# Kernel tuning notes

Hardware: AMD Instinct MI355X
Metric: run time of the kernel (lower is better)

## Reference

```python
import jax, jax.numpy as jnp
import numpy as np
from jax import lax

FPS_NUM, K = 2048, 32


def fps_subsample(x, n):
    # x: [B, N, 3] -> [B, n, 3]; farthest point sampling, deterministic start at index 0
    B, N, _ = x.shape
    d0 = jnp.sum((x - x[:, :1]) ** 2, axis=-1)  # [B, N] dist to point 0

    def step(dists, _):
        nxt = jnp.argmax(dists, axis=1)                       # [B]
        p = x[jnp.arange(B), nxt]                             # [B, 3]
        dists = jnp.minimum(dists, jnp.sum((x - p[:, None]) ** 2, axis=-1))
        return dists, nxt

    _, idxs = lax.scan(step, d0, None, length=n - 1)          # [n-1, B]
    idxs = jnp.concatenate([jnp.zeros((1, B), jnp.int32), idxs.astype(jnp.int32)], axis=0).T  # [B, n]
    return x[jnp.arange(B)[:, None], idxs]                    # [B, n, 3]


def knn_idx(x, k):
    # x: [B, C, N] -> [B, N, k] indices of k nearest neighbors in feature space
    xx = jnp.sum(x * x, axis=1)                               # [B, N]
    inner = jnp.einsum('bcn,bcm->bnm', x, x)
    neg_dist = 2.0 * inner - xx[:, :, None] - xx[:, None, :]  # -||xi-xj||^2
    return lax.top_k(neg_dist, k)[1]


def get_graph_feature(x, k):
    # DGCNN edge features: x [B, C, N] -> [B, 2C, N, k]
    B, C, N = x.shape
    idx = knn_idx(x, k)                                       # [B, N, k]
    xt = jnp.transpose(x, (0, 2, 1))                          # [B, N, C]
    nbr = xt[jnp.arange(B)[:, None, None], idx]               # [B, N, k, C]
    ctr = jnp.broadcast_to(xt[:, :, None], nbr.shape)
    feat = jnp.concatenate([nbr - ctr, ctr], axis=-1)         # [B, N, k, 2C]
    return jnp.transpose(feat, (0, 3, 1, 2))


def attention(xq, xk, pos, Wq, bq, Wk, bk, Wv, bv, Wp, bp):
    # positional attention over k neighbors: xq/xk [B, Cin, N, k], pos [B, 3, N] -> [B, dim, N]
    q = jnp.einsum('bcnk,dc->bdnk', xq, Wq) + bq[:, None, None]
    kk = jnp.einsum('bcnk,dc->bdnk', xk, Wk) + bk[:, None, None]
    v = jnp.einsum('bcnk,dc->bdnk', xk, Wv) + bv[:, None, None]
    p = jnp.einsum('bcn,dc->bdn', pos, Wp) + bp[:, None]      # [B, dim, N]
    dim = Wq.shape[0]
    logits = jnp.einsum('bdnk,bdnk->bnk', q, kk) / jnp.sqrt(jnp.float32(dim))
    attn = jax.nn.softmax(logits, axis=-1)                    # [B, N, k]
    return jnp.einsum('bnk,bdnk->bdn', attn, v + p[:, :, :, None])


def _layer_params(key, cin, dim):
    ks = jax.random.split(key, 4)
    s = 1.0 / np.sqrt(cin)
    return (jax.random.normal(ks[0], (dim, cin), jnp.float32) * s,
            jnp.zeros((dim,), jnp.float32),
            jax.random.normal(ks[1], (dim, cin), jnp.float32) * s,
            jnp.zeros((dim,), jnp.float32),
            jax.random.normal(ks[2], (dim, cin), jnp.float32) * s,
            jnp.zeros((dim,), jnp.float32),
            jax.random.normal(ks[3], (dim, 3), jnp.float32) * (1.0 / np.sqrt(3.0)),
            jnp.zeros((dim,), jnp.float32))


def setup_inputs() -> dict:
    key = jax.random.key(0)
    kx, k1, k2, k3 = jax.random.split(key, 4)
    x = jax.random.normal(kx, (8, 16384, 3), jnp.float32)
    out = {'x': x}
    for name, kk_, cin, dim in (('t1', k1, 6, 64), ('t2', k2, 128, 64), ('t3', k3, 128, 128)):
        Wq, bq, Wk, bk, Wv, bv, Wp, bp = _layer_params(kk_, cin, dim)
        out.update({f'{name}_Wq': Wq, f'{name}_bq': bq, f'{name}_Wk': Wk, f'{name}_bk': bk,
                    f'{name}_Wv': Wv, f'{name}_bv': bv, f'{name}_Wp': Wp, f'{name}_bp': bp})
    return out


def reference(x, t1_Wq, t1_bq, t1_Wk, t1_bk, t1_Wv, t1_bv, t1_Wp, t1_bp,
              t2_Wq, t2_bq, t2_Wk, t2_bk, t2_Wv, t2_bv, t2_Wp, t2_bp,
              t3_Wq, t3_bq, t3_Wk, t3_bk, t3_Wv, t3_bv, t3_Wp, t3_bp):
    partial = jnp.transpose(fps_subsample(x, FPS_NUM), (0, 2, 1))       # [B, 3, n]
    g = get_graph_feature(partial, K)                                    # [B, 6, n, k]
    x1 = attention(g, g, partial, t1_Wq, t1_bq, t1_Wk, t1_bk, t1_Wv, t1_bv, t1_Wp, t1_bp)  # [B, 64, n]
    g = get_graph_feature(x1, K)                                         # [B, 128, n, k]
    x2 = attention(g, g, partial, t2_Wq, t2_bq, t2_Wk, t2_bk, t2_Wv, t2_bv, t2_Wp, t2_bp)  # [B, 64, n]
    g = get_graph_feature(x2, K)                                         # [B, 128, n, k]
    x3 = attention(g, g, partial, t3_Wq, t3_bq, t3_Wk, t3_bk, t3_Wv, t3_bv, t3_Wp, t3_bp)  # [B, 128, n]
    feats = jnp.concatenate([x1, x2, x3], axis=1)                        # [B, 256, n]
    return jnp.concatenate([jnp.max(feats, axis=-1), jnp.mean(feats, axis=-1)], axis=1)    # [B, 512]
```

## Files before the change

### kernel.cpp

```cpp
#include <hip/hip_runtime.h>
#include <math.h>

#define NB 8
#define NIN 16384
#define NP 2048
#define KNN 32
#define TOTPTS (NB * NP)

#define NEG_INF (-__builtin_inff())

template <int CTRL, int RMASK>
__device__ __forceinline__ void dpp_amax_step(float& bv, int& bi) {
  float ov = __int_as_float(__builtin_amdgcn_update_dpp(
      __float_as_int(NEG_INF), __float_as_int(bv), CTRL, RMASK, 0xf, false));
  int oi = __builtin_amdgcn_update_dpp(0, bi, CTRL, RMASK, 0xf, false);
  if (ov > bv || (ov == bv && oi < bi)) { bv = ov; bi = oi; }
}

__device__ __forceinline__ void wave_amax63(float& bv, int& bi) {
  dpp_amax_step<0x111, 0xf>(bv, bi);
  dpp_amax_step<0x112, 0xf>(bv, bi);
  dpp_amax_step<0x114, 0xf>(bv, bi);
  dpp_amax_step<0x118, 0xf>(bv, bi);
  dpp_amax_step<0x142, 0xa>(bv, bi);
  dpp_amax_step<0x143, 0xc>(bv, bi);
}

__global__ __launch_bounds__(1024) void fps_kernel(const float* __restrict__ x,
                                                   float* __restrict__ partial) {
  const int b = blockIdx.x;
  const int t = threadIdx.x;
  const float* xb = x + (size_t)b * NIN * 3;
  float* pb = partial + (size_t)b * NP * 3;
  __shared__ unsigned long long skey[NP];
  for (int i = t; i < NP; i += 1024) skey[i] = 0ull;

  float2 px[8], py[8], pz[8], dd[8];
#pragma unroll
  for (int j = 0; j < 8; ++j) {
    const int i0 = (2 * j) * 1024 + t, i1 = (2 * j + 1) * 1024 + t;
    px[j] = make_float2(xb[3 * i0], xb[3 * i1]);
    py[j] = make_float2(xb[3 * i0 + 1], xb[3 * i1 + 1]);
    pz[j] = make_float2(xb[3 * i0 + 2], xb[3 * i1 + 2]);
  }
  float qx = xb[0], qy = xb[1], qz = xb[2];
  if (t == 0) { pb[0] = qx; pb[1] = qy; pb[2] = qz; }

  float bv = NEG_INF;
  int bi = 0;
#pragma unroll
  for (int j = 0; j < 8; ++j) {
    float dx = __fsub_rn(px[j].x, qx), dy = __fsub_rn(py[j].x, qy), dz = __fsub_rn(pz[j].x, qz);
    dd[j].x = __fadd_rn(__fadd_rn(__fmul_rn(dx, dx), __fmul_rn(dy, dy)), __fmul_rn(dz, dz));
    if (dd[j].x > bv) { bv = dd[j].x; bi = (2 * j) * 1024 + t; }
    dx = __fsub_rn(px[j].y, qx); dy = __fsub_rn(py[j].y, qy); dz = __fsub_rn(pz[j].y, qz);
    dd[j].y = __fadd_rn(__fadd_rn(__fmul_rn(dx, dx), __fmul_rn(dy, dy)), __fmul_rn(dz, dz));
    if (dd[j].y > bv) { bv = dd[j].y; bi = (2 * j + 1) * 1024 + t; }
  }
  __syncthreads();

  for (int it = 1; it < NP; ++it) {
    wave_amax63(bv, bi);
    if ((t & 63) == 63) {
      const unsigned long long key =
          ((unsigned long long)__float_as_uint(bv) << 32) | (unsigned int)(~bi);
      atomicMax(&skey[it], key);
    }
    __syncthreads();
    const unsigned long long gk = skey[it];
    const int gbi = (int)(~(unsigned int)gk);
    const int u = __builtin_amdgcn_readfirstlane(gbi);
    const float nqx = xb[3 * u], nqy = xb[3 * u + 1], nqz = xb[3 * u + 2];
    if (t == 0) { pb[3 * it] = nqx; pb[3 * it + 1] = nqy; pb[3 * it + 2] = nqz; }

    bv = NEG_INF;
    bi = 0;
#pragma unroll
    for (int j = 0; j < 8; ++j) {
      float dx = __fsub_rn(px[j].x, nqx), dy = __fsub_rn(py[j].x, nqy), dz = __fsub_rn(pz[j].x, nqz);
      float nd = __fadd_rn(__fadd_rn(__fmul_rn(dx, dx), __fmul_rn(dy, dy)), __fmul_rn(dz, dz));
      dd[j].x = fminf(dd[j].x, nd);
      if (dd[j].x > bv) { bv = dd[j].x; bi = (2 * j) * 1024 + t; }
      dx = __fsub_rn(px[j].y, nqx); dy = __fsub_rn(py[j].y, nqy); dz = __fsub_rn(pz[j].y, nqz);
      nd = __fadd_rn(__fadd_rn(__fmul_rn(dx, dx), __fmul_rn(dy, dy)), __fmul_rn(dz, dz));
      dd[j].y = fminf(dd[j].y, nd);
      if (dd[j].y > bv) { bv = dd[j].y; bi = (2 * j + 1) * 1024 + t; }
    }
  }
}

__global__ void xx_kernel(const float* __restrict__ F, float* __restrict__ xxg, int C) {
  int i = blockIdx.x * 256 + threadIdx.x;
  if (i >= TOTPTS) return;
  const float* f = F + (size_t)i * C;
  float s = 0.f;
  for (int c = 0; c < C; ++c) s = __fadd_rn(s, __fmul_rn(f[c], f[c]));
  xxg[i] = s;
}

template <int C>
__global__ __launch_bounds__(256) void dist_gemm(const float* __restrict__ F,
                                                 const float* __restrict__ xxg,
                                                 float* __restrict__ D, int bofs) {
  __shared__ float As[64][C + 1];
  __shared__ float Bs[64][C + 1];
  const int b = bofs + blockIdx.z;
  float* Ds = D + (size_t)blockIdx.z * NP * NP;
  const int tid = threadIdx.x;
  const int n0 = blockIdx.y * 64, m0 = blockIdx.x * 64;
  const float* Fb = F + (size_t)b * NP * C;
  const float* xxb = xxg + b * NP;
  for (int t = tid; t < 64 * C; t += 256) {
    int r = t / C, c = t - r * C;
    As[r][c] = Fb[(size_t)(n0 + r) * C + c];
    Bs[r][c] = Fb[(size_t)(m0 + r) * C + c];
  }
  __syncthreads();
  const int tx = tid & 15, ty = tid >> 4;
  float acc[4][4] = {};
  for (int c = 0; c < C; ++c) {
    float a[4], bb[4];
#pragma unroll
    for (int i = 0; i < 4; ++i) a[i] = As[ty * 4 + i][c];
#pragma unroll
    for (int j = 0; j < 4; ++j) bb[j] = Bs[tx * 4 + j][c];
#pragma unroll
    for (int i = 0; i < 4; ++i)
#pragma unroll
      for (int j = 0; j < 4; ++j) acc[i][j] = fmaf(a[i], bb[j], acc[i][j]);
  }
#pragma unroll
  for (int i = 0; i < 4; ++i) {
    int n = n0 + ty * 4 + i;
    float xn = xxb[n];
    float4 o;
    o.x = __fsub_rn(__fsub_rn(2.0f * acc[i][0], xn), xxb[m0 + tx * 4 + 0]);
    o.y = __fsub_rn(__fsub_rn(2.0f * acc[i][1], xn), xxb[m0 + tx * 4 + 1]);
    o.z = __fsub_rn(__fsub_rn(2.0f * acc[i][2], xn), xxb[m0 + tx * 4 + 2]);
    o.w = __fsub_rn(__fsub_rn(2.0f * acc[i][3], xn), xxb[m0 + tx * 4 + 3]);
    *(float4*)&Ds[(size_t)n * NP + m0 + tx * 4] = o;
  }
}

__global__ __launch_bounds__(256) void select_kernel(const float* __restrict__ D,
                                                     int* __restrict__ idxg, int bofs) {
  const int lane = threadIdx.x & 63;
  const int b = bofs + blockIdx.z;
  const int row = blockIdx.x * 4 + (threadIdx.x >> 6);
  const float* Drow = D + (size_t)blockIdx.z * NP * NP + (size_t)row * NP;
  float v[32];
#pragma unroll
  for (int s = 0; s < 32; ++s) v[s] = Drow[s * 64 + lane];
  int* out = idxg + ((size_t)b * NP + row) * KNN;
  for (int t = 0; t < KNN; ++t) {
    float bv = v[0];
    int bs = 0;
#pragma unroll
    for (int s = 1; s < 32; ++s) {
      if (v[s] > bv) { bv = v[s]; bs = s; }
    }
    int bi = bs * 64 + lane;
    wave_amax63(bv, bi);
    const int wbi = __builtin_amdgcn_readlane(bi, 63);
    if (lane == 0) out[t] = wbi;
    const bool own = (lane == (wbi & 63));
    const int cs = wbi >> 6;
#pragma unroll
    for (int s = 0; s < 32; ++s)
      if (own && s == cs) v[s] = NEG_INF;
  }
}

template <int C, int DIM>
__global__ __launch_bounds__(256) void proj_kernel(
    const float* __restrict__ F, const float* __restrict__ pos,
    const float* __restrict__ Wq, const float* __restrict__ bq,
    const float* __restrict__ Wk, const float* __restrict__ bk,
    const float* __restrict__ Wv, const float* __restrict__ bv,
    const float* __restrict__ Wp, const float* __restrict__ bp,
    float* __restrict__ Uq, float* __restrict__ Uk, float* __restrict__ Uv,
    float* __restrict__ Uqc, float* __restrict__ Ukc, float* __restrict__ W6) {
  constexpr int PTS = 16;
  constexpr int GROUPS = 256 / DIM;
  constexpr int PPT = PTS / GROUPS;
  __shared__ float xs[PTS][C];
  __shared__ float ps[PTS][3];
  const int tid = threadIdx.x;
  const int base = blockIdx.x * PTS;
  for (int t = tid; t < PTS * C; t += 256) {
    int r = t / C;
    xs[r][t - r * C] = F[(size_t)(base + r) * C + (t - r * C)];
  }
  for (int t = tid; t < PTS * 3; t += 256) {
    int r = t / 3;
    ps[r][t - r * 3] = pos[(size_t)(base + r) * 3 + (t - r * 3)];
  }
  __syncthreads();
  const int g = tid / DIM;
  const int d = tid - g * DIM;
  float uq[PPT], uqd[PPT], uk[PPT], ukd[PPT], uv[PPT], uvd[PPT];
#pragma unroll
  for (int p = 0; p < PPT; ++p) { uq[p] = uqd[p] = uk[p] = ukd[p] = uv[p] = uvd[p] = 0.f; }
  const float* wqr = Wq + (size_t)d * (2 * C);
  const float* wkr = Wk + (size_t)d * (2 * C);
  const float* wvr = Wv + (size_t)d * (2 * C);
  for (int c = 0; c < C; ++c) {
    const float wq1 = wqr[c], wqd_ = wqr[C + c] - wq1;
    const float wk1 = wkr[c], wkd_ = wkr[C + c] - wk1;
    const float wv1 = wvr[c], wvd_ = wvr[C + c] - wv1;
#pragma unroll
    for (int p = 0; p < PPT; ++p) {
      const float xc = xs[g + p * GROUPS][c];
      uq[p] = fmaf(wq1, xc, uq[p]);
      uqd[p] = fmaf(wqd_, xc, uqd[p]);
      uk[p] = fmaf(wk1, xc, uk[p]);
      ukd[p] = fmaf(wkd_, xc, ukd[p]);
      uv[p] = fmaf(wv1, xc, uv[p]);
      uvd[p] = fmaf(wvd_, xc, uvd[p]);
    }
  }
  const float bqd = bq[d], bkd = bk[d], bvd = bv[d];
  const float wp0 = Wp[d * 3], wp1 = Wp[d * 3 + 1], wp2 = Wp[d * 3 + 2], bpd = bp[d];
#pragma unroll
  for (int p = 0; p < PPT; ++p) {
    const int lp = g + p * GROUPS;
    const size_t o = (size_t)(base + lp) * DIM + d;
    const float pd = wp0 * ps[lp][0] + wp1 * ps[lp][1] + wp2 * ps[lp][2] + bpd;
    Uq[o] = uq[p];
    Uqc[o] = uqd[p] + bqd;
    Uk[o] = uk[p];
    Ukc[o] = ukd[p] + bkd;
    Uv[o] = uv[p];
    W6[o] = uvd[p] + bvd + pd;
  }
}

template <int DIM>
__global__ __launch_bounds__(256) void attn_kernel(
    const float* __restrict__ Uq, const float* __restrict__ Uk, const float* __restrict__ Uv,
    const float* __restrict__ Uqc, const float* __restrict__ Ukc, const float* __restrict__ W6g,
    const int* __restrict__ idxg, float* __restrict__ outF) {
  const int w = threadIdx.x >> 6, lane = threadIdx.x & 63;
  const int pt = blockIdx.x * 4 + w;
  const int b = pt >> 11;
  __shared__ int sidx[4][KNN];
  __shared__ float sqc[4][DIM], skc[4][DIM], sw6[4][DIM];
  __shared__ float sattn[4][KNN];
  const size_t rowo = (size_t)pt * DIM;
  if (lane < KNN) sidx[w][lane] = idxg[(size_t)pt * KNN + lane];
  for (int d = lane; d < DIM; d += 64) {
    sqc[w][d] = Uqc[rowo + d];
    skc[w][d] = Ukc[rowo + d];
    sw6[w][d] = W6g[rowo + d];
  }
  __syncthreads();
  if (lane < KNN) {
    const int ik = sidx[w][lane];
    const float* qr = Uq + (size_t)(b * NP + ik) * DIM;
    const float* kr = Uk + (size_t)(b * NP + ik) * DIM;
    float lg = 0.f;
    for (int d = 0; d < DIM; d += 4) {
      float4 qa = *(const float4*)(qr + d);
      float4 ka = *(const float4*)(kr + d);
      float4 qc = *(const float4*)(&sqc[w][d]);
      float4 kc = *(const float4*)(&skc[w][d]);
      lg += (qa.x + qc.x) * (ka.x + kc.x);
      lg += (qa.y + qc.y) * (ka.y + kc.y);
      lg += (qa.z + qc.z) * (ka.z + kc.z);
      lg += (qa.w + qc.w) * (ka.w + kc.w);
    }
    lg /= sqrtf((float)DIM);
    float m = lg;
#pragma unroll
    for (int off = 16; off; off >>= 1) m = fmaxf(m, __shfl_xor(m, off));
    float e = expf(lg - m);
    float s = e;
#pragma unroll
    for (int off = 16; off; off >>= 1) s += __shfl_xor(s, off);
    sattn[w][lane] = e / s;
  }
  __syncthreads();
  float acc[DIM / 64];
#pragma unroll
  for (int q = 0; q < DIM / 64; ++q) acc[q] = 0.f;
  for (int k = 0; k < KNN; ++k) {
    const int ik = sidx[w][k];
    const float a = sattn[w][k];
    const float* vr = Uv + (size_t)(b * NP + ik) * DIM;
#pragma unroll
    for (int q = 0; q < DIM / 64; ++q) {
      const int d = q * 64 + lane;
      acc[q] = fmaf(a, vr[d] + sw6[w][d], acc[q]);
    }
  }
#pragma unroll
  for (int q = 0; q < DIM / 64; ++q) outF[rowo + q * 64 + lane] = acc[q];
}

__global__ __launch_bounds__(256) void pool_kernel(const float* __restrict__ x1,
                                                   const float* __restrict__ x2,
                                                   const float* __restrict__ x3,
                                                   float* __restrict__ out) {
  const int b = blockIdx.x, c = threadIdx.x;
  const float* src;
  int dim, cl;
  if (c < 64) {
    src = x1 + (size_t)b * NP * 64; dim = 64; cl = c;
  } else if (c < 128) {
    src = x2 + (size_t)b * NP * 64; dim = 64; cl = c - 64;
  } else {
    src = x3 + (size_t)b * NP * 128; dim = 128; cl = c - 128;
  }
  float mx = NEG_INF, sm = 0.f;
#pragma unroll 8
  for (int n = 0; n < NP; ++n) {
    float v = src[(size_t)n * dim + cl];
    mx = fmaxf(mx, v);
    sm += v;
  }
  out[b * 512 + c] = mx;
  out[b * 512 + 256 + c] = sm * (1.0f / 2048.0f);
}

extern "C" void kernel_launch(void* const* d_in, const int* in_sizes, int n_in,
                              void* d_out, int out_size, void* d_ws, size_t ws_size,
                              hipStream_t stream) {
  const float* x = (const float*)d_in[0];
  const float* W[24];
  for (int i = 0; i < 24; ++i) W[i] = (const float*)d_in[1 + i];

  float* ws = (float*)d_ws;
  size_t off = 0;
  float* partial = ws + off; off += (size_t)NB * NP * 3;
  float* xxbuf = ws + off;   off += TOTPTS;
  int* idxb = (int*)(ws + off); off += (size_t)TOTPTS * KNN;
  float* x1 = ws + off; off += (size_t)TOTPTS * 64;
  float* x2 = ws + off; off += (size_t)TOTPTS * 64;
  float* x3 = ws + off; off += (size_t)TOTPTS * 128;
  float* Uq = ws + off;  off += (size_t)TOTPTS * 128;
  float* Uk = ws + off;  off += (size_t)TOTPTS * 128;
  float* Uv = ws + off;  off += (size_t)TOTPTS * 128;
  float* Uqc = ws + off; off += (size_t)TOTPTS * 128;
  float* Ukc = ws + off; off += (size_t)TOTPTS * 128;
  float* W6 = ws + off;  off += (size_t)TOTPTS * 128;
  if (ws_size < off * sizeof(float)) return;

  float* Dbig = ws + off;
  const size_t need_big = (off + (size_t)NB * NP * NP) * sizeof(float);
  const bool bigws = (ws_size >= need_big);
  float* D = bigws ? Dbig : Uq;
  const int NZ = bigws ? NB : 1;

  fps_kernel<<<NB, 1024, 0, stream>>>(x, partial);

  xx_kernel<<<TOTPTS / 256, 256, 0, stream>>>(partial, xxbuf, 3);
  for (int b = 0; b < NB; b += NZ) {
    dist_gemm<3><<<dim3(32, 32, NZ), 256, 0, stream>>>(partial, xxbuf, D, b);
    select_kernel<<<dim3(NP / 4, 1, NZ), 256, 0, stream>>>(D, idxb, b);
  }
  proj_kernel<3, 64><<<TOTPTS / 16, 256, 0, stream>>>(
      partial, partial, W[0], W[1], W[2], W[3], W[4], W[5], W[6], W[7],
      Uq, Uk, Uv, Uqc, Ukc, W6);
  attn_kernel<64><<<TOTPTS / 4, 256, 0, stream>>>(Uq, Uk, Uv, Uqc, Ukc, W6, idxb, x1);

  xx_kernel<<<TOTPTS / 256, 256, 0, stream>>>(x1, xxbuf, 64);
  for (int b = 0; b < NB; b += NZ) {
    dist_gemm<64><<<dim3(32, 32, NZ), 256, 0, stream>>>(x1, xxbuf, D, b);
    select_kernel<<<dim3(NP / 4, 1, NZ), 256, 0, stream>>>(D, idxb, b);
  }
  proj_kernel<64, 64><<<TOTPTS / 16, 256, 0, stream>>>(
      x1, partial, W[8], W[9], W[10], W[11], W[12], W[13], W[14], W[15],
      Uq, Uk, Uv, Uqc, Ukc, W6);
  attn_kernel<64><<<TOTPTS / 4, 256, 0, stream>>>(Uq, Uk, Uv, Uqc, Ukc, W6, idxb, x2);

  xx_kernel<<<TOTPTS / 256, 256, 0, stream>>>(x2, xxbuf, 64);
  for (int b = 0; b < NB; b += NZ) {
    dist_gemm<64><<<dim3(32, 32, NZ), 256, 0, stream>>>(x2, xxbuf, D, b);
    select_kernel<<<dim3(NP / 4, 1, NZ), 256, 0, stream>>>(D, idxb, b);
  }
  proj_kernel<64, 128><<<TOTPTS / 16, 256, 0, stream>>>(
      x2, partial, W[16], W[17], W[18], W[19], W[20], W[21], W[22], W[23],
      Uq, Uk, Uv, Uqc, Ukc, W6);
  attn_kernel<128><<<TOTPTS / 4, 256, 0, stream>>>(Uq, Uk, Uv, Uqc, Ukc, W6, idxb, x3);

  pool_kernel<<<NB, 256, 0, stream>>>(x1, x2, x3, (float*)d_out);
}
```

Measured before the change: 5.517 ms.

## Pack FPS math, split argmax reduction, GEMM-based projections, two-half attention logits

The FPS inner loop switches to packed v_pk_add/v_pk_mul float2 arithmetic, and the wave argmax becomes a float max followed by an index min instead of paired value/index DPP steps. For layers 2 and 3, the per-point projection kernel is replaced by a weight-prep kernel, a positional kernel and a tiled shared-memory GEMM that emits all six projection outputs at once. Attention logits now use all 64 lanes, each half-wave covering half the channels, and a constant replaces the sqrt divide. These changes target the serial FPS loop and the cost of the projections, at the price of extra launches, extra workspace and slightly different rounding.

```diff
diff --git a/kernel.cpp b/kernel.cpp
--- a/kernel.cpp
+++ b/kernel.cpp
@@ -9,14 +9,47 @@
 
 #define NEG_INF (-__builtin_inff())
 
+__device__ __forceinline__ float2 pk_add(float2 a, float2 b) {
+  float2 d;
+  asm("v_pk_add_f32 %0, %1, %2" : "=v"(d) : "v"(a), "v"(b));
+  return d;
+}
+__device__ __forceinline__ float2 pk_mul(float2 a, float2 b) {
+  float2 d;
+  asm("v_pk_mul_f32 %0, %1, %2" : "=v"(d) : "v"(a), "v"(b));
+  return d;
+}
+
+#define DPP_F(old, v, C, RM) \
+  __int_as_float(__builtin_amdgcn_update_dpp(__float_as_int(old), __float_as_int(v), C, RM, 0xf, false))
+#define DPP_I(old, v, C, RM) \
+  __builtin_amdgcn_update_dpp(old, v, C, RM, 0xf, false)
+
+__device__ __forceinline__ float wave_max_f(float v) {
+  v = fmaxf(v, DPP_F(NEG_INF, v, 0x111, 0xf));
+  v = fmaxf(v, DPP_F(NEG_INF, v, 0x112, 0xf));
+  v = fmaxf(v, DPP_F(NEG_INF, v, 0x114, 0xf));
+  v = fmaxf(v, DPP_F(NEG_INF, v, 0x118, 0xf));
+  v = fmaxf(v, DPP_F(NEG_INF, v, 0x142, 0xa));
+  v = fmaxf(v, DPP_F(NEG_INF, v, 0x143, 0xc));
+  return v;
+}
+__device__ __forceinline__ int wave_min_i(int v) {
+  v = min(v, DPP_I(0x7fffffff, v, 0x111, 0xf));
+  v = min(v, DPP_I(0x7fffffff, v, 0x112, 0xf));
+  v = min(v, DPP_I(0x7fffffff, v, 0x114, 0xf));
+  v = min(v, DPP_I(0x7fffffff, v, 0x118, 0xf));
+  v = min(v, DPP_I(0x7fffffff, v, 0x142, 0xa));
+  v = min(v, DPP_I(0x7fffffff, v, 0x143, 0xc));
+  return v;
+}
+
 template <int CTRL, int RMASK>
 __device__ __forceinline__ void dpp_amax_step(float& bv, int& bi) {
-  float ov = __int_as_float(__builtin_amdgcn_update_dpp(
-      __float_as_int(NEG_INF), __float_as_int(bv), CTRL, RMASK, 0xf, false));
-  int oi = __builtin_amdgcn_update_dpp(0, bi, CTRL, RMASK, 0xf, false);
+  float ov = DPP_F(NEG_INF, bv, CTRL, RMASK);
+  int oi = DPP_I(0, bi, CTRL, RMASK);
   if (ov > bv || (ov == bv && oi < bi)) { bv = ov; bi = oi; }
 }
-
 __device__ __forceinline__ void wave_amax63(float& bv, int& bi) {
   dpp_amax_step<0x111, 0xf>(bv, bi);
   dpp_amax_step<0x112, 0xf>(bv, bi);
@@ -43,27 +76,34 @@
     py[j] = make_float2(xb[3 * i0 + 1], xb[3 * i1 + 1]);
     pz[j] = make_float2(xb[3 * i0 + 2], xb[3 * i1 + 2]);
   }
-  float qx = xb[0], qy = xb[1], qz = xb[2];
-  if (t == 0) { pb[0] = qx; pb[1] = qy; pb[2] = qz; }
+  const float qx0 = xb[0], qy0 = xb[1], qz0 = xb[2];
+  if (t == 0) { pb[0] = qx0; pb[1] = qy0; pb[2] = qz0; }
 
   float bv = NEG_INF;
   int bi = 0;
-#pragma unroll
-  for (int j = 0; j < 8; ++j) {
-    float dx = __fsub_rn(px[j].x, qx), dy = __fsub_rn(py[j].x, qy), dz = __fsub_rn(pz[j].x, qz);
-    dd[j].x = __fadd_rn(__fadd_rn(__fmul_rn(dx, dx), __fmul_rn(dy, dy)), __fmul_rn(dz, dz));
-    if (dd[j].x > bv) { bv = dd[j].x; bi = (2 * j) * 1024 + t; }
-    dx = __fsub_rn(px[j].y, qx); dy = __fsub_rn(py[j].y, qy); dz = __fsub_rn(pz[j].y, qz);
-    dd[j].y = __fadd_rn(__fadd_rn(__fmul_rn(dx, dx), __fmul_rn(dy, dy)), __fmul_rn(dz, dz));
-    if (dd[j].y > bv) { bv = dd[j].y; bi = (2 * j + 1) * 1024 + t; }
+  {
+    const float2 nx2 = make_float2(-qx0, -qx0);
+    const float2 ny2 = make_float2(-qy0, -qy0);
+    const float2 nz2 = make_float2(-qz0, -qz0);
+#pragma unroll
+    for (int j = 0; j < 8; ++j) {
+      float2 dx = pk_add(px[j], nx2), dy = pk_add(py[j], ny2), dz = pk_add(pz[j], nz2);
+      float2 nd = pk_add(pk_add(pk_mul(dx, dx), pk_mul(dy, dy)), pk_mul(dz, dz));
+      dd[j] = nd;
+      if (nd.x > bv) { bv = nd.x; bi = (2 * j) * 1024 + t; }
+      if (nd.y > bv) { bv = nd.y; bi = (2 * j + 1) * 1024 + t; }
+    }
   }
   __syncthreads();
 
   for (int it = 1; it < NP; ++it) {
-    wave_amax63(bv, bi);
+    const float wm = wave_max_f(bv);
+    const float smax = __int_as_float(__builtin_amdgcn_readlane(__float_as_int(wm), 63));
+    const int sel = (bv == smax) ? bi : 0x7fffffff;
+    const int wi = wave_min_i(sel);
     if ((t & 63) == 63) {
       const unsigned long long key =
-          ((unsigned long long)__float_as_uint(bv) << 32) | (unsigned int)(~bi);
+          ((unsigned long long)__float_as_uint(smax) << 32) | (unsigned int)(~wi);
       atomicMax(&skey[it], key);
     }
     __syncthreads();
@@ -73,18 +113,21 @@
     const float nqx = xb[3 * u], nqy = xb[3 * u + 1], nqz = xb[3 * u + 2];
     if (t == 0) { pb[3 * it] = nqx; pb[3 * it + 1] = nqy; pb[3 * it + 2] = nqz; }
 
+    const float2 nx2 = make_float2(-nqx, -nqx);
+    const float2 ny2 = make_float2(-nqy, -nqy);
+    const float2 nz2 = make_float2(-nqz, -nqz);
     bv = NEG_INF;
     bi = 0;
 #pragma unroll
     for (int j = 0; j < 8; ++j) {
-      float dx = __fsub_rn(px[j].x, nqx), dy = __fsub_rn(py[j].x, nqy), dz = __fsub_rn(pz[j].x, nqz);
-      float nd = __fadd_rn(__fadd_rn(__fmul_rn(dx, dx), __fmul_rn(dy, dy)), __fmul_rn(dz, dz));
-      dd[j].x = fminf(dd[j].x, nd);
-      if (dd[j].x > bv) { bv = dd[j].x; bi = (2 * j) * 1024 + t; }
-      dx = __fsub_rn(px[j].y, nqx); dy = __fsub_rn(py[j].y, nqy); dz = __fsub_rn(pz[j].y, nqz);
-      nd = __fadd_rn(__fadd_rn(__fmul_rn(dx, dx), __fmul_rn(dy, dy)), __fmul_rn(dz, dz));
-      dd[j].y = fminf(dd[j].y, nd);
-      if (dd[j].y > bv) { bv = dd[j].y; bi = (2 * j + 1) * 1024 + t; }
+      float2 dx = pk_add(px[j], nx2), dy = pk_add(py[j], ny2), dz = pk_add(pz[j], nz2);
+      float2 nd = pk_add(pk_add(pk_mul(dx, dx), pk_mul(dy, dy)), pk_mul(dz, dz));
+      const float a0 = fminf(dd[j].x, nd.x);
+      dd[j].x = a0;
+      if (a0 > bv) { bv = a0; bi = (2 * j) * 1024 + t; }
+      const float a1 = fminf(dd[j].y, nd.y);
+      dd[j].y = a1;
+      if (a1 > bv) { bv = a1; bi = (2 * j + 1) * 1024 + t; }
     }
   }
 }
@@ -236,6 +279,87 @@
 }
 
 template <int DIM>
+__global__ void prep_kernel(const float* __restrict__ Wq, const float* __restrict__ bq,
+                            const float* __restrict__ Wk, const float* __restrict__ bk,
+                            const float* __restrict__ Wv, const float* __restrict__ bv,
+                            float* __restrict__ Wcat, float* __restrict__ bcat) {
+  const int o = blockIdx.x * 256 + threadIdx.x;
+  constexpr int ND = 6 * DIM;
+  if (o >= ND) return;
+  const int blk = o / DIM, d = o % DIM;
+  bcat[o] = (blk == 1) ? bq[d] : (blk == 3) ? bk[d] : (blk == 5) ? bv[d] : 0.f;
+  const float* W = (blk < 2) ? Wq : (blk < 4) ? Wk : Wv;
+  for (int c = 0; c < 64; ++c) {
+    const float w1 = W[(size_t)d * 128 + c];
+    const float w2 = W[(size_t)d * 128 + 64 + c];
+    Wcat[(size_t)c * ND + o] = (blk & 1) ? (w2 - w1) : w1;
+  }
+}
+
+template <int DIM>
+__global__ void pos_kernel(const float* __restrict__ pos, const float* __restrict__ Wp,
+                           const float* __restrict__ bp, float* __restrict__ P) {
+  const int idx = blockIdx.x * 256 + threadIdx.x;
+  const int pt = idx / DIM, d = idx - pt * DIM;
+  P[idx] = Wp[d * 3] * pos[pt * 3] + Wp[d * 3 + 1] * pos[pt * 3 + 1] +
+           Wp[d * 3 + 2] * pos[pt * 3 + 2] + bp[d];
+}
+
+template <int DIM>
+__global__ __launch_bounds__(256) void gemm_proj(
+    const float* __restrict__ F, const float* __restrict__ Wcat,
+    const float* __restrict__ bcat, const float* __restrict__ P,
+    float* __restrict__ Uq, float* __restrict__ Uqc, float* __restrict__ Uk,
+    float* __restrict__ Ukc, float* __restrict__ Uv, float* __restrict__ W6) {
+  constexpr int ND = 6 * DIM;
+  __shared__ float As[64][65];
+  __shared__ float Bs[64][65];
+  const int tid = threadIdx.x;
+  const int p0 = blockIdx.x * 64;
+  const int n0 = blockIdx.y * 64;
+  {
+    const int r0 = tid >> 4, c4 = (tid & 15) * 4;
+    for (int r = r0; r < 64; r += 16) {
+      float4 a = *(const float4*)&F[(size_t)(p0 + r) * 64 + c4];
+      As[r][c4] = a.x; As[r][c4 + 1] = a.y; As[r][c4 + 2] = a.z; As[r][c4 + 3] = a.w;
+      float4 bb = *(const float4*)&Wcat[(size_t)r * ND + n0 + c4];
+      Bs[r][c4] = bb.x; Bs[r][c4 + 1] = bb.y; Bs[r][c4 + 2] = bb.z; Bs[r][c4 + 3] = bb.w;
+    }
+  }
+  __syncthreads();
+  const int tx = tid & 15, ty = tid >> 4;
+  float acc[4][4] = {};
+#pragma unroll 4
+  for (int c = 0; c < 64; ++c) {
+    float a[4], bb[4];
+#pragma unroll
+    for (int i = 0; i < 4; ++i) a[i] = As[ty * 4 + i][c];
+#pragma unroll
+    for (int j = 0; j < 4; ++j) bb[j] = Bs[c][tx * 4 + j];
+#pragma unroll
+    for (int i = 0; i < 4; ++i)
+#pragma unroll
+      for (int j = 0; j < 4; ++j) acc[i][j] = fmaf(a[i], bb[j], acc[i][j]);
+  }
+  const int obuf = n0 / DIM;
+  const int oloc = n0 - obuf * DIM;
+  float* outp = (obuf == 0) ? Uq : (obuf == 1) ? Uqc : (obuf == 2) ? Uk
+              : (obuf == 3) ? Ukc : (obuf == 4) ? Uv : W6;
+  const float b0 = bcat[n0 + tx * 4], b1 = bcat[n0 + tx * 4 + 1];
+  const float b2 = bcat[n0 + tx * 4 + 2], b3 = bcat[n0 + tx * 4 + 3];
+#pragma unroll
+  for (int i = 0; i < 4; ++i) {
+    const int p = p0 + ty * 4 + i;
+    float4 r = make_float4(acc[i][0] + b0, acc[i][1] + b1, acc[i][2] + b2, acc[i][3] + b3);
+    if (obuf == 5) {
+      float4 pv = *(const float4*)&P[(size_t)p * DIM + oloc + tx * 4];
+      r.x += pv.x; r.y += pv.y; r.z += pv.z; r.w += pv.w;
+    }
+    *(float4*)&outp[(size_t)p * DIM + oloc + tx * 4] = r;
+  }
+}
+
+template <int DIM>
 __global__ __launch_bounds__(256) void attn_kernel(
     const float* __restrict__ Uq, const float* __restrict__ Uk, const float* __restrict__ Uv,
     const float* __restrict__ Uqc, const float* __restrict__ Ukc, const float* __restrict__ W6g,
@@ -254,12 +378,15 @@
     sw6[w][d] = W6g[rowo + d];
   }
   __syncthreads();
-  if (lane < KNN) {
-    const int ik = sidx[w][lane];
+  {
+    const int kk = lane & 31;
+    const int h = lane >> 5;
+    const int ik = sidx[w][kk];
     const float* qr = Uq + (size_t)(b * NP + ik) * DIM;
     const float* kr = Uk + (size_t)(b * NP + ik) * DIM;
     float lg = 0.f;
-    for (int d = 0; d < DIM; d += 4) {
+    const int d0 = h * (DIM / 2), d1 = d0 + DIM / 2;
+    for (int d = d0; d < d1; d += 4) {
       float4 qa = *(const float4*)(qr + d);
       float4 ka = *(const float4*)(kr + d);
       float4 qc = *(const float4*)(&sqc[w][d]);
@@ -269,7 +396,8 @@
       lg += (qa.z + qc.z) * (ka.z + kc.z);
       lg += (qa.w + qc.w) * (ka.w + kc.w);
     }
-    lg /= sqrtf((float)DIM);
+    lg += __shfl_xor(lg, 32);
+    lg *= (DIM == 64) ? 0.125f : 0.08838834764831845f;
     float m = lg;
 #pragma unroll
     for (int off = 16; off; off >>= 1) m = fmaxf(m, __shfl_xor(m, off));
@@ -277,7 +405,7 @@
     float s = e;
 #pragma unroll
     for (int off = 16; off; off >>= 1) s += __shfl_xor(s, off);
-    sattn[w][lane] = e / s;
+    if (lane < KNN) sattn[w][lane] = e / s;
   }
   __syncthreads();
   float acc[DIM / 64];
@@ -343,6 +471,9 @@
   float* Uqc = ws + off; off += (size_t)TOTPTS * 128;
   float* Ukc = ws + off; off += (size_t)TOTPTS * 128;
   float* W6 = ws + off;  off += (size_t)TOTPTS * 128;
+  float* Pbuf = ws + off; off += (size_t)TOTPTS * 128;
+  float* Wcat = ws + off; off += (size_t)64 * 768;
+  float* bcat = ws + off; off += 768;
   if (ws_size < off * sizeof(float)) return;
 
   float* Dbig = ws + off;
@@ -368,9 +499,10 @@
     dist_gemm<64><<<dim3(32, 32, NZ), 256, 0, stream>>>(x1, xxbuf, D, b);
     select_kernel<<<dim3(NP / 4, 1, NZ), 256, 0, stream>>>(D, idxb, b);
   }
-  proj_kernel<64, 64><<<TOTPTS / 16, 256, 0, stream>>>(
-      x1, partial, W[8], W[9], W[10], W[11], W[12], W[13], W[14], W[15],
-      Uq, Uk, Uv, Uqc, Ukc, W6);
+  prep_kernel<64><<<2, 256, 0, stream>>>(W[8], W[9], W[10], W[11], W[12], W[13], Wcat, bcat);
+  pos_kernel<64><<<TOTPTS * 64 / 256, 256, 0, stream>>>(partial, W[14], W[15], Pbuf);
+  gemm_proj<64><<<dim3(TOTPTS / 64, 6), 256, 0, stream>>>(
+      x1, Wcat, bcat, Pbuf, Uq, Uqc, Uk, Ukc, Uv, W6);
   attn_kernel<64><<<TOTPTS / 4, 256, 0, stream>>>(Uq, Uk, Uv, Uqc, Ukc, W6, idxb, x2);
 
   xx_kernel<<<TOTPTS / 256, 256, 0, stream>>>(x2, xxbuf, 64);
@@ -378,9 +510,10 @@
     dist_gemm<64><<<dim3(32, 32, NZ), 256, 0, stream>>>(x2, xxbuf, D, b);
     select_kernel<<<dim3(NP / 4, 1, NZ), 256, 0, stream>>>(D, idxb, b);
   }
-  proj_kernel<64, 128><<<TOTPTS / 16, 256, 0, stream>>>(
-      x2, partial, W[16], W[17], W[18], W[19], W[20], W[21], W[22], W[23],
-      Uq, Uk, Uv, Uqc, Ukc, W6);
+  prep_kernel<128><<<3, 256, 0, stream>>>(W[16], W[17], W[18], W[19], W[20], W[21], Wcat, bcat);
+  pos_kernel<128><<<TOTPTS * 128 / 256, 256, 0, stream>>>(partial, W[22], W[23], Pbuf);
+  gemm_proj<128><<<dim3(TOTPTS / 64, 12), 256, 0, stream>>>(
+      x2, Wcat, bcat, Pbuf, Uq, Uqc, Uk, Ukc, Uv, W6);
   attn_kernel<128><<<TOTPTS / 4, 256, 0, stream>>>(Uq, Uk, Uv, Uqc, Ukc, W6, idxb, x3);
 
   pool_kernel<<<NB, 256, 0, stream>>>(x1, x2, x3, (float*)d_out);
```

New measurement: 4.816 ms. -12.7%, faster.
